# Kernel tuning notes

Measured on AMD Instinct MI355X. Metric: run time of the kernel, lower is better.

The kernel has to match this reference:

```python
import jax, jax.numpy as jnp
import numpy as np

TAU = 0.05


def setup_inputs() -> dict:
    key = jax.random.key(0)
    ks = jax.random.split(key, 4)
    N, D, F, E = 8192, 1024, 4096, 8
    h = jax.random.normal(ks[0], (N, D), dtype=jnp.float32)
    Wr = jax.random.normal(ks[1], (D, E), dtype=jnp.float32) * (1.0 / np.sqrt(D))
    br = jnp.zeros((E,), dtype=jnp.float32)
    W1 = jax.random.normal(ks[2], (E, D, F), dtype=jnp.float32) * (1.0 / np.sqrt(D))
    b1 = jnp.zeros((E, F), dtype=jnp.float32)
    W2 = jax.random.normal(ks[3], (E, F, D), dtype=jnp.float32) * (1.0 / np.sqrt(F))
    b2 = jnp.zeros((E, D), dtype=jnp.float32)
    return {"h": h, "Wr": Wr, "br": br, "W1": W1, "b1": b1, "W2": W2, "b2": b2}


def reference(h, Wr, br, W1, b1, W2, b2):
    # Router: linear + softmax over experts -> [N, E]
    weights = jax.nn.softmax(h @ Wr + br, axis=-1)
    # Threshold mask (weights > tau); masked_weights = weights * mask
    masked_w = jnp.where(weights > TAU, weights, 0.0)  # [N, E]
    # Experts: 2-layer MLP per expert, computed batched over the expert axis.
    # hid: [N, E, F]
    hid = jax.nn.gelu(jnp.einsum('nd,edf->nef', h, W1) + b1)
    # expert outputs: [N, E, D]
    out_e = jnp.einsum('nef,efd->ned', hid, W2) + b2
    # Weighted combine; zero masked weights annihilate inactive experts,
    # matching the conditional sum (and the zeros_like fallback when none active).
    return jnp.einsum('ne,ned->nd', masked_w, out_e)
```

## Files before the change

kernel.cpp:

```cpp
#include <hip/hip_runtime.h>
#include <hip/hip_bf16.h>
#include <cstdint>
#include <cstddef>

typedef __attribute__((ext_vector_type(8))) __bf16 bf16x8;
typedef __attribute__((ext_vector_type(4))) float f32x4;
typedef __attribute__((ext_vector_type(4))) unsigned short us4;

#define GLOAD_LDS16(g, l)                                                        \
    __builtin_amdgcn_global_load_lds(                                            \
        (const __attribute__((address_space(1))) void*)(g),                      \
        (__attribute__((address_space(3))) void*)(l), 16, 0, 0)

static __device__ __forceinline__ unsigned short f2bf(float x) {
    unsigned int u = __builtin_bit_cast(unsigned int, x);
    return (unsigned short)((u + 0x7FFFu + ((u >> 16) & 1u)) >> 16);
}

static __device__ __forceinline__ float gelu_fast(float x) {
    const float p = x * x;
    const float u = x * fmaf(0.0713548162726f, p, 1.59576912161f);
    const float t = __expf(-u);
    return x * __builtin_amdgcn_rcpf(1.0f + t);
}

__global__ __launch_bounds__(256) void moe_router_kernel(
    const float* __restrict__ h, const float* __restrict__ Wr,
    const float* __restrict__ br, unsigned short* __restrict__ hbf,
    float* __restrict__ mw)
{
    const int lane = threadIdx.x & 63, wave = threadIdx.x >> 6;
    const int n = blockIdx.x * 4 + wave;
    const float* hr = h + (size_t)n * 1024;
    const int base = lane * 16;

    float xs[16];
#pragma unroll
    for (int q = 0; q < 4; ++q) {
        f32x4 v = *(const f32x4*)(hr + base + q * 4);
        xs[q * 4 + 0] = v[0]; xs[q * 4 + 1] = v[1];
        xs[q * 4 + 2] = v[2]; xs[q * 4 + 3] = v[3];
    }
    float acc[8] = {0.f, 0.f, 0.f, 0.f, 0.f, 0.f, 0.f, 0.f};
#pragma unroll
    for (int j = 0; j < 16; ++j) {
        const float x = xs[j];
        const f32x4 w0 = *(const f32x4*)(Wr + (size_t)(base + j) * 8);
        const f32x4 w1 = *(const f32x4*)(Wr + (size_t)(base + j) * 8 + 4);
        acc[0] += x * w0[0]; acc[1] += x * w0[1]; acc[2] += x * w0[2]; acc[3] += x * w0[3];
        acc[4] += x * w1[0]; acc[5] += x * w1[1]; acc[6] += x * w1[2]; acc[7] += x * w1[3];
    }
#pragma unroll
    for (int q = 0; q < 4; ++q) {
        us4 o;
        o[0] = f2bf(xs[q * 4 + 0]); o[1] = f2bf(xs[q * 4 + 1]);
        o[2] = f2bf(xs[q * 4 + 2]); o[3] = f2bf(xs[q * 4 + 3]);
        *(us4*)(hbf + (size_t)n * 1024 + base + q * 4) = o;
    }
#pragma unroll
    for (int m = 32; m >= 1; m >>= 1)
#pragma unroll
        for (int e = 0; e < 8; ++e) acc[e] += __shfl_xor(acc[e], m, 64);

    if (lane == 0) {
        float l[8]; float mx = -1e30f;
#pragma unroll
        for (int e = 0; e < 8; ++e) { l[e] = acc[e] + br[e]; mx = fmaxf(mx, l[e]); }
        float s = 0.f;
#pragma unroll
        for (int e = 0; e < 8; ++e) { l[e] = __expf(l[e] - mx); s += l[e]; }
        const float inv = 1.0f / s;
#pragma unroll
        for (int e = 0; e < 8; ++e) {
            const float w = l[e] * inv;
            mw[(size_t)n * 8 + e] = (w > 0.05f) ? w : 0.0f;
        }
    }
}

__global__ __launch_bounds__(256) void moe_tcvt_kernel(
    const float* __restrict__ in, unsigned short* __restrict__ out,
    int ls, size_t in_es, int os, size_t out_es)
{
    __shared__ unsigned short t[32][33];
    const int e = blockIdx.z;
    const int r = threadIdx.x >> 3, c = (threadIdx.x & 7) * 4;
    const float* I = in + (size_t)e * in_es + (size_t)(blockIdx.x * 32 + r) * ls + blockIdx.y * 32 + c;
    f32x4 v = *(const f32x4*)I;
    t[r][c + 0] = f2bf(v[0]); t[r][c + 1] = f2bf(v[1]);
    t[r][c + 2] = f2bf(v[2]); t[r][c + 3] = f2bf(v[3]);
    __syncthreads();
    unsigned short* O = out + (size_t)e * out_es + (size_t)(blockIdx.y * 32 + r) * os + blockIdx.x * 32 + c;
    us4 o;
    o[0] = t[c + 0][r]; o[1] = t[c + 1][r]; o[2] = t[c + 2][r]; o[3] = t[c + 3][r];
    *(us4*)O = o;
}

#define MFMA_QUAD(MB, NB, AF, BQ)                                              \
  _Pragma("unroll") for (int mi_ = 0; mi_ < 4; ++mi_)                          \
  _Pragma("unroll") for (int ni_ = 0; ni_ < 2; ++ni_) {                        \
      acc[(MB)+mi_][(NB)+ni_] = __builtin_amdgcn_mfma_f32_16x16x32_bf16(       \
          BQ[ni_][1], AF[mi_][1], __builtin_amdgcn_mfma_f32_16x16x32_bf16(     \
          BQ[ni_][0], AF[mi_][0], acc[(MB)+mi_][(NB)+ni_], 0, 0, 0), 0, 0, 0); \
  }

#define PH_MID()  do { __builtin_amdgcn_s_barrier();                           \
    asm volatile("s_waitcnt lgkmcnt(0)" ::: "memory");                         \
    __builtin_amdgcn_sched_barrier(0);                                         \
    __builtin_amdgcn_s_setprio(1); } while (0)
#define PH_ENDQ() do { __builtin_amdgcn_s_setprio(0);                          \
    __builtin_amdgcn_s_barrier(); } while (0)

template <int MODE>
__global__ __launch_bounds__(512) void moe_gemm8p(
    const unsigned short* __restrict__ A, int ldga,
    const unsigned short* __restrict__ Bbase, size_t estride, int ldb,
    const float* __restrict__ b1, const float* __restrict__ mw,
    unsigned short* __restrict__ Cg, int ldc,
    float* __restrict__ part,
    int logFc, int f0glob, int kspan, int init)
{
    __shared__ unsigned short sh[65536];
    char* sm = (char*)sh;
    const int XA = 0, XB = 32768, YA = 65536, YB = 98304;

    const int tid = threadIdx.x, lane = tid & 63, wv = tid >> 6;
    const int wr = wv >> 2, wc = wv & 3;

    int bx, by;
    if constexpr (MODE == 0) {
        const int gy = gridDim.y;
        const int orig = blockIdx.x + blockIdx.y * 32;
        const int c8 = orig & 7, j = orig >> 3;
        bx = c8 * 4 + j / gy; by = j % gy;
    } else {
        const int orig = blockIdx.x + blockIdx.y * 32;
        const int c8 = orig & 7, j = orig >> 3;
        bx = c8 * 4 + (j >> 2); by = j & 3;
    }
    const int m0 = bx * 256;
    const int n0 = by * 256;

    const int z = (MODE == 1) ? blockIdx.z : 0;
    const int klo = z * kspan;
    float* Cacc = (MODE == 1) ? part + (size_t)z * (8192 * 1024) : nullptr;

    int e0 = 0, fb = 0;
    const unsigned short* gB0 = nullptr;
    const int rl0 = tid >> 3;
    const int gs8 = ((tid & 7) ^ (rl0 & 7)) * 8;
    if constexpr (MODE == 0) {
        e0 = n0 >> logFc; fb = n0 - (e0 << logFc);
        gB0 = Bbase + (size_t)e0 * estride + (size_t)(fb + rl0) * ldb + gs8;
    }
    const unsigned short* gA0 = A + (size_t)(m0 + rl0) * ldga + gs8;
    const int dstw = wv * 1024;

    auto stage_tile = [&](int regA, int regB, int kk) {
        const unsigned short* ga = gA0 + kk;
        const unsigned short* gb;
        if constexpr (MODE == 0) {
            gb = gB0 + kk;
        } else {
            const int e = kk >> logFc, kc = kk - (e << logFc);
            gb = Bbase + (size_t)e * estride + (size_t)(n0 + rl0) * ldb + kc + gs8;
        }
#pragma unroll
        for (int hf = 0; hf < 2; ++hf)
#pragma unroll
            for (int q = 0; q < 2; ++q) {
                const int rr = hf * 128 + q * 64;
                GLOAD_LDS16(ga + (size_t)rr * ldga, sm + regA + hf * 16384 + q * 8192 + dstw);
                GLOAD_LDS16(gb + (size_t)rr * ldb,  sm + regB + hf * 16384 + q * 8192 + dstw);
            }
    };

    const int l15 = lane & 15, l4 = lane >> 4, l7 = lane & 7;
    const int sA0 = (wr * 128 + l15) * 128 + (((0 + l4) ^ l7) << 4);
    const int sA1 = (wr * 128 + l15) * 128 + (((4 + l4) ^ l7) << 4);
    const int sB0 = (wc * 64 + l15) * 128 + (((0 + l4) ^ l7) << 4);
    const int sB1 = (wc * 64 + l15) * 128 + (((4 + l4) ^ l7) << 4);

    f32x4 acc[8][4] = {};
    bf16x8 afL[4][2], afH[4][2], bqL[2][2], bqH[2][2];

#define RD_AFL(BASE) _Pragma("unroll") for (int mi_=0;mi_<4;++mi_){            \
      afL[mi_][0] = *(const bf16x8*)(sm + (BASE) + sA0 + mi_*2048);            \
      afL[mi_][1] = *(const bf16x8*)(sm + (BASE) + sA1 + mi_*2048); }
#define RD_AFH(BASE) _Pragma("unroll") for (int mi_=0;mi_<4;++mi_){            \
      afH[mi_][0] = *(const bf16x8*)(sm + (BASE) + sA0 + (4+mi_)*2048);        \
      afH[mi_][1] = *(const bf16x8*)(sm + (BASE) + sA1 + (4+mi_)*2048); }
#define RD_BQL(BASE) _Pragma("unroll") for (int ni_=0;ni_<2;++ni_){            \
      bqL[ni_][0] = *(const bf16x8*)(sm + (BASE) + sB0 + ni_*2048);            \
      bqL[ni_][1] = *(const bf16x8*)(sm + (BASE) + sB1 + ni_*2048); }
#define RD_BQH(BASE) _Pragma("unroll") for (int ni_=0;ni_<2;++ni_){            \
      bqH[ni_][0] = *(const bf16x8*)(sm + (BASE) + sB0 + (2+ni_)*2048);        \
      bqH[ni_][1] = *(const bf16x8*)(sm + (BASE) + sB1 + (2+ni_)*2048); }

    const int niter = kspan >> 7;

    stage_tile(XA, XB, klo);
    stage_tile(YA, YB, klo + 64);
    asm volatile("s_waitcnt vmcnt(8)" ::: "memory");
    __builtin_amdgcn_sched_barrier(0);
    __builtin_amdgcn_s_barrier();

    for (int it = 0; it < niter; ++it) {
        const int kkX = klo + it * 128;
        const bool g = (it + 1 < niter);
        RD_AFL(XA); RD_BQL(XB);
        PH_MID(); MFMA_QUAD(0, 0, afL, bqL); PH_ENDQ();
        RD_BQH(XB);
        PH_MID(); MFMA_QUAD(0, 2, afL, bqH); PH_ENDQ();
        RD_AFH(XA);
        PH_MID(); MFMA_QUAD(4, 0, afH, bqL); PH_ENDQ();
        if (g) { stage_tile(XA, XB, kkX + 128);
                 asm volatile("s_waitcnt vmcnt(8)" ::: "memory"); }
        else   { asm volatile("s_waitcnt vmcnt(0)" ::: "memory"); }
        __builtin_amdgcn_sched_barrier(0);
        __builtin_amdgcn_s_barrier();
        __builtin_amdgcn_s_setprio(1);
        MFMA_QUAD(4, 2, afH, bqH);
        PH_ENDQ();
        RD_AFL(YA); RD_BQL(YB);
        PH_MID(); MFMA_QUAD(0, 0, afL, bqL); PH_ENDQ();
        RD_BQH(YB);
        PH_MID(); MFMA_QUAD(0, 2, afL, bqH); PH_ENDQ();
        RD_AFH(YA);
        PH_MID(); MFMA_QUAD(4, 0, afH, bqL); PH_ENDQ();
        if (g) { stage_tile(YA, YB, kkX + 192);
                 asm volatile("s_waitcnt vmcnt(8)" ::: "memory"); }
        else   { asm volatile("s_waitcnt vmcnt(0)" ::: "memory"); }
        __builtin_amdgcn_sched_barrier(0);
        __builtin_amdgcn_s_barrier();
        __builtin_amdgcn_s_setprio(1);
        MFMA_QUAD(4, 2, afH, bqH);
        PH_ENDQ();
    }

    const int nr0v = l4 * 4;
    if constexpr (MODE == 0) {
        const float* b1p = b1 + (size_t)e0 * 4096 + f0glob + fb;
        f32x4 b1v[4];
#pragma unroll
        for (int j = 0; j < 4; ++j)
            b1v[j] = *(const f32x4*)(b1p + wc * 64 + j * 16 + nr0v);
#pragma unroll
        for (int i = 0; i < 8; ++i) {
            const int token = m0 + wr * 128 + i * 16 + l15;
            const float w = mw[(size_t)token * 8 + e0];
            unsigned short* crow = Cg + (size_t)token * ldc + n0;
#pragma unroll
            for (int j = 0; j < 4; ++j) {
                const int n = wc * 64 + j * 16 + nr0v;
                us4 o;
#pragma unroll
                for (int r = 0; r < 4; ++r)
                    o[r] = f2bf(w * gelu_fast(acc[i][j][r] + b1v[j][r]));
                *(us4*)(crow + n) = o;
            }
        }
    } else {
#pragma unroll
        for (int i = 0; i < 8; ++i) {
            const int row = m0 + wr * 128 + i * 16 + l15;
            float* cp = Cacc + (size_t)row * 1024 + n0;
#pragma unroll
            for (int j = 0; j < 4; ++j) {
                const int n = wc * 64 + j * 16 + nr0v;
                if (init) {
                    *(f32x4*)(cp + n) = acc[i][j];
                } else {
                    f32x4 old = *(const f32x4*)(cp + n);
                    *(f32x4*)(cp + n) = old + acc[i][j];
                }
            }
        }
    }
}

__global__ __launch_bounds__(256) void moe_combine_kernel(
    const float* __restrict__ part, int S,
    float* __restrict__ out, const float* __restrict__ mw,
    const float* __restrict__ b2)
{
    const int n = blockIdx.x, t = threadIdx.x;
    const int d = t * 4;
    f32x4 v = *(const f32x4*)(part + (size_t)n * 1024 + d);
    for (int z = 1; z < S; ++z)
        v = v + *(const f32x4*)(part + (size_t)z * (8192 * 1024) + (size_t)n * 1024 + d);
#pragma unroll
    for (int e = 0; e < 8; ++e) {
        const float w = mw[(size_t)n * 8 + e];
        const f32x4 b = *(const f32x4*)(b2 + (size_t)e * 1024 + d);
        v = v + w * b;
    }
    *(f32x4*)(out + (size_t)n * 1024 + d) = v;
}

extern "C" void kernel_launch(void* const* d_in, const int* in_sizes, int n_in,
                              void* d_out, int out_size, void* d_ws, size_t ws_size,
                              hipStream_t stream)
{
    (void)in_sizes; (void)n_in; (void)out_size;
    const float* h  = (const float*)d_in[0];
    const float* Wr = (const float*)d_in[1];
    const float* br = (const float*)d_in[2];
    const float* W1 = (const float*)d_in[3];
    const float* b1 = (const float*)d_in[4];
    const float* W2 = (const float*)d_in[5];
    const float* b2 = (const float*)d_in[6];
    float* out = (float*)d_out;

    const int N = 8192, D = 1024, F = 4096, E = 8;
    const int S = 2;
    auto al = [](size_t x) { return (x + 255) & ~(size_t)255; };
    const size_t sz_hbf = al((size_t)N * D * 2);
    const size_t sz_mw  = al((size_t)N * E * 4);
    const size_t sz_pt1 = al((size_t)N * D * 4);
    auto tot = [&](int fc, bool full) {
        size_t s = sz_hbf + sz_mw + al((size_t)N * ((size_t)E * fc + 64) * 2);
        s += (full ? al((size_t)E * F * D * 2) : al((size_t)E * fc * D * 2)) * 2;
        s += (size_t)S * sz_pt1;
        return s;
    };
    int Fc; bool full;
    if      (tot(512, true)  <= ws_size) { Fc = 512; full = true;  }
    else if (tot(512, false) <= ws_size) { Fc = 512; full = false; }
    else                                 { Fc = 256; full = false; }
    const int logFc = (Fc == 512) ? 9 : 8;
    const int Kc = E * Fc;
    const int ldAp = Kc + 64;

    char* p = (char*)d_ws;
    unsigned short* hbf = (unsigned short*)p; p += sz_hbf;
    float* mwp  = (float*)p; p += sz_mw;
    unsigned short* ghid = (unsigned short*)p; p += al((size_t)N * (size_t)ldAp * 2);
    unsigned short* W1t  = (unsigned short*)p;
    p += full ? al((size_t)E * F * D * 2) : al((size_t)E * Fc * D * 2);
    unsigned short* W2t  = (unsigned short*)p;
    p += full ? al((size_t)E * F * D * 2) : al((size_t)E * Fc * D * 2);
    float* part = (float*)p;

    moe_router_kernel<<<N / 4, 256, 0, stream>>>(h, Wr, br, hbf, mwp);

    if (full) {
        moe_tcvt_kernel<<<dim3(D / 32, F / 32, E), 256, 0, stream>>>(
            W1, W1t, F, (size_t)D * F, D, (size_t)F * D);
        moe_tcvt_kernel<<<dim3(F / 32, D / 32, E), 256, 0, stream>>>(
            W2, W2t, D, (size_t)F * D, F, (size_t)D * F);
    }

    const int nch = F / Fc;
    for (int c = 0; c < nch; ++c) {
        if (!full) {
            moe_tcvt_kernel<<<dim3(D / 32, Fc / 32, E), 256, 0, stream>>>(
                W1 + (size_t)c * Fc, W1t, F, (size_t)D * F, D, (size_t)Fc * D);
            moe_tcvt_kernel<<<dim3(Fc / 32, D / 32, E), 256, 0, stream>>>(
                W2 + (size_t)c * Fc * D, W2t, D, (size_t)F * D, Fc, (size_t)D * Fc);
        }
        const unsigned short* B1p = W1t + (full ? (size_t)c * Fc * D : 0);
        const size_t es1 = full ? (size_t)F * D : (size_t)Fc * D;
        moe_gemm8p<0><<<dim3(32, Kc / 256, 1), 512, 0, stream>>>(
            hbf, 1024, B1p, es1, 1024, b1, mwp, ghid, ldAp, nullptr,
            logFc, c * Fc, 1024, 0);

        const unsigned short* B2p = W2t + (full ? (size_t)c * Fc : 0);
        const size_t es2 = full ? (size_t)D * F : (size_t)D * Fc;
        const int ldb2 = full ? F : Fc;
        moe_gemm8p<1><<<dim3(32, 4, S), 512, 0, stream>>>(
            ghid, ldAp, B2p, es2, ldb2, nullptr, nullptr, nullptr, 0, part,
            logFc, 0, Kc / S, (c == 0) ? 1 : 0);
    }

    moe_combine_kernel<<<N, 256, 0, stream>>>(part, S, out, mwp, b2);
}
```

Measured before the change: 1.525 ms.

## Interleave global-to-LDS loads across MFMA phases and prefetch LDS fragments

Splits the per-tile global_load_lds staging into per-quarter A and B loads and spreads them across the four MFMA phases, issuing each quarter once the LDS rows it overwrites have been read into registers. LDS fragment reads for the next phase are issued before the current phase's MFMAs, and the barriers use partial lgkmcnt waits, so ds_reads overlap matrix work. The aim is to hide LDS and global latency and smooth memory traffic across the main loop. The hazard reasoning is now spread across several hand-placed waits and barriers, so an ordering slip could corrupt data, and there are more barriers per iteration.

```diff
diff --git a/kernel.cpp b/kernel.cpp
--- a/kernel.cpp
+++ b/kernel.cpp
@@ -104,12 +104,12 @@
           BQ[ni_][0], AF[mi_][0], acc[(MB)+mi_][(NB)+ni_], 0, 0, 0), 0, 0, 0); \
   }
 
-#define PH_MID()  do { __builtin_amdgcn_s_barrier();                           \
-    asm volatile("s_waitcnt lgkmcnt(0)" ::: "memory");                         \
-    __builtin_amdgcn_sched_barrier(0);                                         \
-    __builtin_amdgcn_s_setprio(1); } while (0)
-#define PH_ENDQ() do { __builtin_amdgcn_s_setprio(0);                          \
-    __builtin_amdgcn_s_barrier(); } while (0)
+#define BARX()   __builtin_amdgcn_s_barrier()
+#define SBX()    __builtin_amdgcn_sched_barrier(0)
+#define LGKM(N)  asm volatile("s_waitcnt lgkmcnt(" #N ")" ::: "memory")
+#define VMC(N)   asm volatile("s_waitcnt vmcnt(" #N ")" ::: "memory")
+#define PRIO1()  __builtin_amdgcn_s_setprio(1)
+#define PRIO0()  __builtin_amdgcn_s_setprio(0)
 
 template <int MODE>
 __global__ __launch_bounds__(512) void moe_gemm8p(
@@ -156,8 +156,11 @@
     const unsigned short* gA0 = A + (size_t)(m0 + rl0) * ldga + gs8;
     const int dstw = wv * 1024;
 
-    auto stage_tile = [&](int regA, int regB, int kk) {
-        const unsigned short* ga = gA0 + kk;
+    auto stageA = [&](int reg, int kk, int q) {
+        GLOAD_LDS16(gA0 + kk + (size_t)(q * 64) * ldga,
+                    sm + reg + (q >> 1) * 16384 + (q & 1) * 8192 + dstw);
+    };
+    auto stageB = [&](int reg, int kk, int q) {
         const unsigned short* gb;
         if constexpr (MODE == 0) {
             gb = gB0 + kk;
@@ -165,14 +168,8 @@
             const int e = kk >> logFc, kc = kk - (e << logFc);
             gb = Bbase + (size_t)e * estride + (size_t)(n0 + rl0) * ldb + kc + gs8;
         }
-#pragma unroll
-        for (int hf = 0; hf < 2; ++hf)
-#pragma unroll
-            for (int q = 0; q < 2; ++q) {
-                const int rr = hf * 128 + q * 64;
-                GLOAD_LDS16(ga + (size_t)rr * ldga, sm + regA + hf * 16384 + q * 8192 + dstw);
-                GLOAD_LDS16(gb + (size_t)rr * ldb,  sm + regB + hf * 16384 + q * 8192 + dstw);
-            }
+        GLOAD_LDS16(gb + (size_t)(q * 64) * ldb,
+                    sm + reg + (q >> 1) * 16384 + (q & 1) * 8192 + dstw);
     };
 
     const int l15 = lane & 15, l4 = lane >> 4, l7 = lane & 7;
@@ -199,43 +196,46 @@
 
     const int niter = kspan >> 7;
 
-    stage_tile(XA, XB, klo);
-    stage_tile(YA, YB, klo + 64);
-    asm volatile("s_waitcnt vmcnt(8)" ::: "memory");
-    __builtin_amdgcn_sched_barrier(0);
-    __builtin_amdgcn_s_barrier();
+#pragma unroll
+    for (int q = 0; q < 4; ++q) { stageA(XA, klo, q); stageB(XB, klo, q); }
+#pragma unroll
+    for (int q = 0; q < 4; ++q) { stageA(YA, klo + 64, q); stageB(YB, klo + 64, q); }
+    VMC(8); SBX();
+    BARX();
+    RD_AFL(XA); RD_BQL(XB);
 
     for (int it = 0; it < niter; ++it) {
-        const int kkX = klo + it * 128;
+        const int kX2 = klo + it * 128 + 128;
+        const int kY2 = klo + it * 128 + 192;
         const bool g = (it + 1 < niter);
-        RD_AFL(XA); RD_BQL(XB);
-        PH_MID(); MFMA_QUAD(0, 0, afL, bqL); PH_ENDQ();
         RD_BQH(XB);
-        PH_MID(); MFMA_QUAD(0, 2, afL, bqH); PH_ENDQ();
+        BARX(); LGKM(4); SBX(); PRIO1(); MFMA_QUAD(0, 0, afL, bqL); PRIO0(); BARX();
         RD_AFH(XA);
-        PH_MID(); MFMA_QUAD(4, 0, afH, bqL); PH_ENDQ();
-        if (g) { stage_tile(XA, XB, kkX + 128);
-                 asm volatile("s_waitcnt vmcnt(8)" ::: "memory"); }
-        else   { asm volatile("s_waitcnt vmcnt(0)" ::: "memory"); }
-        __builtin_amdgcn_sched_barrier(0);
-        __builtin_amdgcn_s_barrier();
-        __builtin_amdgcn_s_setprio(1);
-        MFMA_QUAD(4, 2, afH, bqH);
-        PH_ENDQ();
+        if (g) { stageA(XA, kX2, 0); stageA(XA, kX2, 2); }
+        BARX(); LGKM(8); SBX(); PRIO1(); MFMA_QUAD(0, 2, afL, bqH); PRIO0(); BARX();
+        if (g) { stageB(XB, kX2, 0); stageB(XB, kX2, 1); }
+        BARX(); LGKM(0); SBX(); PRIO1(); MFMA_QUAD(4, 0, afH, bqL); PRIO0(); BARX();
+        if (g) { stageA(XA, kX2, 1); stageA(XA, kX2, 3);
+                 stageB(XB, kX2, 2); stageB(XB, kX2, 3);
+                 VMC(8); } else { VMC(0); }
+        SBX();
+        BARX();
         RD_AFL(YA); RD_BQL(YB);
-        PH_MID(); MFMA_QUAD(0, 0, afL, bqL); PH_ENDQ();
+        SBX(); PRIO1(); MFMA_QUAD(4, 2, afH, bqH); PRIO0(); BARX();
         RD_BQH(YB);
-        PH_MID(); MFMA_QUAD(0, 2, afL, bqH); PH_ENDQ();
+        BARX(); LGKM(4); SBX(); PRIO1(); MFMA_QUAD(0, 0, afL, bqL); PRIO0(); BARX();
         RD_AFH(YA);
-        PH_MID(); MFMA_QUAD(4, 0, afH, bqL); PH_ENDQ();
-        if (g) { stage_tile(YA, YB, kkX + 192);
-                 asm volatile("s_waitcnt vmcnt(8)" ::: "memory"); }
-        else   { asm volatile("s_waitcnt vmcnt(0)" ::: "memory"); }
-        __builtin_amdgcn_sched_barrier(0);
-        __builtin_amdgcn_s_barrier();
-        __builtin_amdgcn_s_setprio(1);
-        MFMA_QUAD(4, 2, afH, bqH);
-        PH_ENDQ();
+        if (g) { stageA(YA, kY2, 0); stageA(YA, kY2, 2); }
+        BARX(); LGKM(8); SBX(); PRIO1(); MFMA_QUAD(0, 2, afL, bqH); PRIO0(); BARX();
+        if (g) { stageB(YB, kY2, 0); stageB(YB, kY2, 1); }
+        BARX(); LGKM(0); SBX(); PRIO1(); MFMA_QUAD(4, 0, afH, bqL); PRIO0(); BARX();
+        if (g) { stageA(YA, kY2, 1); stageA(YA, kY2, 3);
+                 stageB(YB, kY2, 2); stageB(YB, kY2, 3);
+                 VMC(8); } else { VMC(0); }
+        SBX();
+        BARX();
+        if (g) { RD_AFL(XA); RD_BQL(XB); }
+        SBX(); PRIO1(); MFMA_QUAD(4, 2, afH, bqH); PRIO0(); BARX();
     }
 
     const int nr0v = l4 * 4;
```

After: 1.359 ms. -10.9%, faster.
